# Performance work log

Measured on AMD Instinct MI355X. Metric: run time of the kernel, lower is better.

## Reference

```python
import jax, jax.numpy as jnp
import numpy as np

DIM = 512
SEQ_LEN = 1279
IMG = 32
K = 7
DIL = 1
H = 8
DH = 64
INNER = H * DH


def _unfold(x, k, pad, dil, pad_value=0.0):
    # x: [B, C, Hh, Ww] -> [B, Hh*Ww, k*k, C]  (torch F.unfold channel order: c outer, kernel inner)
    B, C, Hh, Ww = x.shape
    xp = jnp.pad(x, ((0, 0), (0, 0), (pad, pad), (pad, pad)), constant_values=pad_value)
    cols = [xp[:, :, i * dil:i * dil + Hh, j * dil:j * dil + Ww]
            for i in range(k) for j in range(k)]
    p = jnp.stack(cols, axis=2)  # [B, C, k*k, Hh, Ww]
    return p.reshape(B, C, k * k, Hh * Ww).transpose(0, 3, 2, 1)


def setup_inputs() -> dict:
    key = jax.random.key(0)
    ks = jax.random.split(key, 3)
    b = 4
    x = jax.random.normal(ks[0], (b, SEQ_LEN, DIM), jnp.float32)
    mask = jnp.ones((b, 256), dtype=bool)
    W_qkv = jax.random.normal(ks[1], (DIM, INNER * 3), jnp.float32) * 0.02
    W_out = jax.random.normal(ks[2], (INNER, DIM), jnp.float32) * 0.02
    b_out = jnp.zeros((DIM,), jnp.float32)
    return {"x": x, "mask": mask, "W_qkv": W_qkv, "W_out": W_out, "b_out": b_out}


def reference(x, mask, W_qkv, W_out, b_out):
    b, n, _ = x.shape
    img_seq_len = IMG * IMG                      # 1024
    text_len = SEQ_LEN + 1 - img_seq_len         # 256
    pad_n = SEQ_LEN - n + 1                      # pad to seq_len + 1
    scale = DH ** -0.5

    xp = jnp.pad(x, ((0, 0), (0, pad_n), (0, 0)))
    mask = mask[:, :text_len]

    qkv = xp @ W_qkv
    q, k, v = jnp.split(qkv, 3, axis=-1)

    def split_heads(t):
        B, N, _ = t.shape
        return t.reshape(B, N, H, DH).transpose(0, 2, 1, 3).reshape(B * H, N, DH)

    q, k, v = map(split_heads, (q, k, v))
    q = q * scale

    q_text, q_img = q[:, :-img_seq_len], q[:, -img_seq_len:]
    k_text, k_img = k[:, :-img_seq_len], k[:, -img_seq_len:]
    v_text, v_img = v[:, :-img_seq_len], v[:, -img_seq_len:]

    # --- text-to-text causal attention ---
    dots_text = jnp.einsum('bid,bjd->bij', q_text, k_text)
    mask_value = -jnp.finfo(dots_text.dtype).max
    i, j = dots_text.shape[-2:]
    causal_text = jnp.triu(jnp.ones((i, j), dtype=bool), j - i + 1)
    dots_text = jnp.where(causal_text, mask_value, dots_text)
    attn_text = jax.nn.softmax(dots_text, axis=-1)
    out_text = jnp.einsum('bij,bjd->bid', attn_text, v_text)

    # --- image local windowed attention (unfold) + image-to-text ---
    eff = (K - 1) * DIL + 1
    pad = eff // 2

    def to_img(t):
        B = t.shape[0]
        return t.transpose(0, 2, 1).reshape(B, DH, IMG, IMG)

    k_imgu = _unfold(to_img(k_img), K, pad, DIL)  # [BH, HW, KK, DH]
    v_imgu = _unfold(to_img(v_img), K, pad, DIL)

    dots_image = jnp.einsum('bid,bijd->bij', q_img, k_imgu)
    dots_i2t = jnp.einsum('bid,bjd->bij', q_img, k_text)

    img_seq = jnp.arange(img_seq_len, dtype=jnp.float32).reshape(1, 1, IMG, IMG)
    k_idx = _unfold(img_seq, K, pad, DIL, pad_value=float(img_seq_len))[..., 0]  # [1, HW, KK]
    q_idx = jnp.arange(img_seq_len)[None, :, None]
    causal_img = q_idx < k_idx  # [1, HW, KK]

    bh = q.shape[0]
    causal_img = jnp.broadcast_to(causal_img, (bh, img_seq_len, K * K))
    tmask = jnp.broadcast_to(mask[:, None, None, :], (b, H, img_seq_len, text_len)).reshape(bh, img_seq_len, text_len)
    full_mask = jnp.concatenate((~tmask, causal_img), axis=-1)

    dots = jnp.concatenate((dots_i2t, dots_image), axis=-1)
    dots = jnp.where(full_mask, mask_value, dots)
    attn = jax.nn.softmax(dots, axis=-1)
    attn_i2t, attn_img = attn[..., :text_len], attn[..., text_len:]

    out_img = (jnp.einsum('bij,bijd->bid', attn_img, v_imgu)
               + jnp.einsum('bij,bjd->bid', attn_i2t, v_text))

    out = jnp.concatenate((out_text, out_img), axis=1)  # [BH, N, DH]
    N = out.shape[1]
    out = out.reshape(b, H, N, DH).transpose(0, 2, 1, 3).reshape(b, N, INNER)
    out = out @ W_out + b_out
    return out[:, :n]
```

## Files before the change

kernel.cpp:

```cpp
#include <hip/hip_runtime.h>
#include <math.h>

#define DIMD 512
#define SEQ 1280
#define NREAL 1279
#define NTEXT 256
#define NIMG 1024
#define IMGW 32
#define NH 8
#define DH 64
#define BH 32
#define BATCH 4
#define VTW 1344
#define FLTMAX 3.402823466e38f

typedef __attribute__((ext_vector_type(8))) short short8;
typedef __attribute__((ext_vector_type(4))) float f32x4;
typedef __attribute__((ext_vector_type(4))) unsigned short ushort4v;
typedef __attribute__((ext_vector_type(8))) unsigned short ushort8v;

#define MFMA16(a, b, c) __builtin_amdgcn_mfma_f32_16x16x32_bf16((a), (b), (c), 0, 0, 0)

__device__ __forceinline__ unsigned short f2bf(float x) {
    unsigned int u = __builtin_bit_cast(unsigned int, x);
    u += 0x7fffu + ((u >> 16) & 1u);
    return (unsigned short)(u >> 16);
}

__device__ __forceinline__ void gload16(const unsigned short* g, unsigned short* l) {
    __builtin_amdgcn_global_load_lds(
        (const __attribute__((address_space(1))) unsigned int*)g,
        (__attribute__((address_space(3))) unsigned int*)l,
        16, 0, 0);
}

__global__ __launch_bounds__(256) void convert_fused(
    const float* __restrict__ x, const float* __restrict__ Wqkv,
    const float* __restrict__ Wout, unsigned short* __restrict__ xb,
    unsigned short* __restrict__ wqkvt, unsigned short* __restrict__ woutt)
{
    __shared__ unsigned short lds[64 * 65];
    const int blk = blockIdx.x;
    const int t = threadIdx.x;

    if (blk < 1280) {
        const size_t tt = (size_t)blk * 256 + t;
        const size_t e0 = tt * 8;
        const int row = (int)(e0 >> 9);
        const int d = (int)(e0 & 511);
        const int b = row / SEQ;
        const int ns = row - b * SEQ;
        ushort8v o;
        if (ns < NREAL) {
            const float4* p = reinterpret_cast<const float4*>(
                x + ((size_t)b * NREAL + ns) * DIMD + d);
            float4 v0 = p[0], v1 = p[1];
            o[0] = f2bf(v0.x); o[1] = f2bf(v0.y); o[2] = f2bf(v0.z); o[3] = f2bf(v0.w);
            o[4] = f2bf(v1.x); o[5] = f2bf(v1.y); o[6] = f2bf(v1.z); o[7] = f2bf(v1.w);
        } else {
            o = ushort8v{0, 0, 0, 0, 0, 0, 0, 0};
        }
        *reinterpret_cast<ushort8v*>(xb + e0) = o;
        return;
    }

    const bool isq = (blk < 1472);
    const int lb = blk - (isq ? 1280 : 1472);
    const float* W = isq ? Wqkv : Wout;
    unsigned short* Wt = isq ? wqkvt : woutt;
    const int N = isq ? 1536 : 512;
    const int k0 = (lb & 7) * 64, n0 = (lb >> 3) * 64;

    #pragma unroll
    for (int i = 0; i < 4; i++) {
        int idx = t + 256 * i;
        int r = idx >> 4, c4 = (idx & 15) * 4;
        float4 v = *reinterpret_cast<const float4*>(W + (size_t)(k0 + r) * N + n0 + c4);
        lds[(c4 + 0) * 65 + r] = f2bf(v.x);
        lds[(c4 + 1) * 65 + r] = f2bf(v.y);
        lds[(c4 + 2) * 65 + r] = f2bf(v.z);
        lds[(c4 + 3) * 65 + r] = f2bf(v.w);
    }
    __syncthreads();
    #pragma unroll
    for (int i = 0; i < 4; i++) {
        int idx = t + 256 * i;
        int n = idx >> 4, k4 = (idx & 15) * 4;
        ushort4v o;
        #pragma unroll
        for (int j = 0; j < 4; j++) o[j] = lds[n * 65 + k4 + j];
        *reinterpret_cast<ushort4v*>(Wt + (size_t)(n0 + n) * 512 + k0 + k4) = o;
    }
}

template<int TM, int TN, int EPI>
__global__ __launch_bounds__(256) void mfma_gemm(
    const unsigned short* __restrict__ A, const unsigned short* __restrict__ Bt,
    unsigned short* __restrict__ qb, unsigned short* __restrict__ kb,
    unsigned short* __restrict__ vt,
    const float* __restrict__ bias, float* __restrict__ out)
{
    constexpr int MI = TM / 32;
    constexpr int NI = TN / 32;
    __shared__ __align__(16) unsigned short As[TM * 64];
    __shared__ __align__(16) unsigned short Bs[TN * 64];
    const int tid = threadIdx.x;
    const int lane = tid & 63, w = tid >> 6;
    const int wm = w >> 1, wn = w & 1;
    const int g = lane >> 4, col = lane & 15;
    const int m0 = blockIdx.x * TM, n0 = blockIdx.y * TN;
    char* AsB = (char*)&As[0];
    char* BsB = (char*)&Bs[0];

    f32x4 acc[MI][NI] = {};

    for (int ks = 0; ks < 8; ks++) {
        const int k0 = ks * 64;
        #pragma unroll
        for (int j = 0; j < TM / 32; j++) {
            int rbase = w * (TM / 4) + j * 8;
            int r = rbase + (lane >> 3);
            int cs = (lane & 7) ^ (r & 7);
            gload16(A + (size_t)(m0 + r) * 512 + k0 + cs * 8,
                    (unsigned short*)(AsB + rbase * 128));
        }
        #pragma unroll
        for (int j = 0; j < TN / 32; j++) {
            int rbase = w * (TN / 4) + j * 8;
            int r = rbase + (lane >> 3);
            int cs = (lane & 7) ^ (r & 7);
            gload16(Bt + (size_t)(n0 + r) * 512 + k0 + cs * 8,
                    (unsigned short*)(BsB + rbase * 128));
        }
        __syncthreads();

        short8 af[MI][2], bfr[NI][2];
        #pragma unroll
        for (int mi = 0; mi < MI; mi++) {
            int rA = wm * (TM / 2) + mi * 16 + col;
            #pragma unroll
            for (int kk = 0; kk < 2; kk++) {
                int sl = (kk * 4 + g) ^ (rA & 7);
                af[mi][kk] = *reinterpret_cast<const short8*>(AsB + rA * 128 + sl * 16);
            }
        }
        #pragma unroll
        for (int ni = 0; ni < NI; ni++) {
            int rB = wn * (TN / 2) + ni * 16 + col;
            #pragma unroll
            for (int kk = 0; kk < 2; kk++) {
                int sl = (kk * 4 + g) ^ (rB & 7);
                bfr[ni][kk] = *reinterpret_cast<const short8*>(BsB + rB * 128 + sl * 16);
            }
        }
        #pragma unroll
        for (int kk = 0; kk < 2; kk++)
            #pragma unroll
            for (int mi = 0; mi < MI; mi++)
                #pragma unroll
                for (int ni = 0; ni < NI; ni++)
                    acc[mi][ni] = MFMA16(af[mi][kk], bfr[ni][kk], acc[mi][ni]);
        __syncthreads();
    }

    const int b = m0 / SEQ;
    const int nb = m0 - b * SEQ;

    if (EPI == 0) {
        #pragma unroll
        for (int ni = 0; ni < NI; ni++) {
            const int n = n0 + wn * (TN / 2) + ni * 16 + col;
            const int which = n >> 9;
            const int h = (n >> 6) & 7;
            const int dh = n & 63;
            const int bh = b * NH + h;
            #pragma unroll
            for (int mi = 0; mi < MI; mi++) {
                const int ns0 = nb + wm * (TM / 2) + mi * 16 + 4 * g;
                if (which == 2) {
                    ushort4v pk;
                    #pragma unroll
                    for (int rr = 0; rr < 4; rr++) pk[rr] = f2bf(acc[mi][ni][rr]);
                    *reinterpret_cast<ushort4v*>(
                        vt + ((size_t)bh * DH + dh) * VTW + ns0) = pk;
                } else {
                    unsigned short* dst = which ? kb : qb;
                    const float sc = which ? 1.f : 0.125f;
                    #pragma unroll
                    for (int rr = 0; rr < 4; rr++)
                        dst[((size_t)bh * SEQ + ns0 + rr) * DH + dh] =
                            f2bf(acc[mi][ni][rr] * sc);
                }
            }
        }
    } else {
        #pragma unroll
        for (int ni = 0; ni < NI; ni++) {
            const int n = n0 + wn * (TN / 2) + ni * 16 + col;
            const float bv = bias[n];
            #pragma unroll
            for (int mi = 0; mi < MI; mi++) {
                const int ns0 = nb + wm * (TM / 2) + mi * 16 + 4 * g;
                #pragma unroll
                for (int rr = 0; rr < 4; rr++) {
                    int ns = ns0 + rr;
                    if (ns < NREAL)
                        out[((size_t)b * NREAL + ns) * DIMD + n] = acc[mi][ni][rr] + bv;
                }
            }
        }
    }
}

__device__ __forceinline__ void attn_text_body(
    const unsigned short* __restrict__ qb, const unsigned short* __restrict__ kb,
    const unsigned short* __restrict__ vt, unsigned short* __restrict__ ao,
    unsigned short* P, int bh, int t, int lane)
{
    const int g = lane >> 4, col = lane & 15;
    const int b = bh >> 3, h = bh & 7;

    const size_t qrow = (size_t)bh * SEQ + t * 16 + col;
    const short8 qa0 = *reinterpret_cast<const short8*>(qb + qrow * DH + g * 8);
    const short8 qa1 = *reinterpret_cast<const short8*>(qb + qrow * DH + 32 + g * 8);

    f32x4 st[16];
    #pragma unroll
    for (int kt = 0; kt < 16; kt++) {
        if (kt <= t) {
            size_t krow = (size_t)bh * SEQ + kt * 16 + col;
            short8 kb0 = *reinterpret_cast<const short8*>(kb + krow * DH + g * 8);
            short8 kb1 = *reinterpret_cast<const short8*>(kb + krow * DH + 32 + g * 8);
            f32x4 s = {0.f, 0.f, 0.f, 0.f};
            s = MFMA16(qa0, kb0, s);
            s = MFMA16(qa1, kb1, s);
            if (kt == t) {
                #pragma unroll
                for (int rr = 0; rr < 4; rr++)
                    if (col > 4 * g + rr) s[rr] = -FLTMAX;
            }
            st[kt] = s;
        }
    }

    float m[4] = {-FLTMAX, -FLTMAX, -FLTMAX, -FLTMAX};
    #pragma unroll
    for (int kt = 0; kt < 16; kt++)
        if (kt <= t)
            #pragma unroll
            for (int rr = 0; rr < 4; rr++) m[rr] = fmaxf(m[rr], st[kt][rr]);
    #pragma unroll
    for (int rr = 0; rr < 4; rr++) {
        m[rr] = fmaxf(m[rr], __shfl_xor(m[rr], 1));
        m[rr] = fmaxf(m[rr], __shfl_xor(m[rr], 2));
        m[rr] = fmaxf(m[rr], __shfl_xor(m[rr], 4));
        m[rr] = fmaxf(m[rr], __shfl_xor(m[rr], 8));
    }
    float ssum[4] = {0.f, 0.f, 0.f, 0.f};
    #pragma unroll
    for (int kt = 0; kt < 16; kt++)
        if (kt <= t) {
            #pragma unroll
            for (int rr = 0; rr < 4; rr++) {
                float e = __expf(st[kt][rr] - m[rr]);
                st[kt][rr] = e;
                ssum[rr] += e;
            }
        }
    #pragma unroll
    for (int rr = 0; rr < 4; rr++) {
        ssum[rr] += __shfl_xor(ssum[rr], 1);
        ssum[rr] += __shfl_xor(ssum[rr], 2);
        ssum[rr] += __shfl_xor(ssum[rr], 4);
        ssum[rr] += __shfl_xor(ssum[rr], 8);
    }

    #pragma unroll
    for (int kt = 0; kt < 16; kt++)
        if (kt <= t) {
            #pragma unroll
            for (int rr = 0; rr < 4; rr++)
                P[(4 * g + rr) * 264 + kt * 16 + col] = f2bf(st[kt][rr]);
        }
    if ((t & 1) == 0) {
        ushort4v z = {0, 0, 0, 0};
        *reinterpret_cast<ushort4v*>(
            &P[(lane >> 2) * 264 + (t + 1) * 16 + (lane & 3) * 4]) = z;
    }
    __syncthreads();

    f32x4 acc[4] = {};
    #pragma unroll
    for (int kkb = 0; kkb < 8; kkb++) {
        if (kkb <= (t >> 1)) {
            short8 pa = *reinterpret_cast<const short8*>(&P[col * 264 + kkb * 32 + g * 8]);
            #pragma unroll
            for (int n0t = 0; n0t < 4; n0t++) {
                short8 vb = *reinterpret_cast<const short8*>(
                    vt + ((size_t)bh * DH + n0t * 16 + col) * VTW + kkb * 32 + g * 8);
                acc[n0t] = MFMA16(pa, vb, acc[n0t]);
            }
        }
    }

    #pragma unroll
    for (int rr = 0; rr < 4; rr++) {
        int qrow_o = t * 16 + 4 * g + rr;
        float inv = 1.f / ssum[rr];
        #pragma unroll
        for (int n0t = 0; n0t < 4; n0t++)
            ao[((size_t)b * SEQ + qrow_o) * DIMD + h * DH + n0t * 16 + col] =
                f2bf(acc[n0t][rr] * inv);
    }
}

__device__ __forceinline__ void attn_img_body(
    const unsigned short* __restrict__ qb, const unsigned short* __restrict__ kb,
    const unsigned short* __restrict__ vt, const int* __restrict__ mask,
    unsigned short* __restrict__ ao, unsigned short* P, int bh, int tile, int lane)
{
    const int r = tile >> 1, c0 = (tile & 1) << 4;
    const int g = lane >> 4, col = lane & 15;
    const int b = bh >> 3, h = bh & 7;

    const size_t qrow = (size_t)bh * SEQ + NTEXT + r * 32 + c0 + col;
    const short8 qa0 = *reinterpret_cast<const short8*>(qb + qrow * DH + g * 8);
    const short8 qa1 = *reinterpret_cast<const short8*>(qb + qrow * DH + 32 + g * 8);

    f32x4 st[16];
    #pragma unroll
    for (int kt = 0; kt < 16; kt++) {
        int j = kt * 16 + col;
        size_t krow = (size_t)bh * SEQ + j;
        short8 kb0 = *reinterpret_cast<const short8*>(kb + krow * DH + g * 8);
        short8 kb1 = *reinterpret_cast<const short8*>(kb + krow * DH + 32 + g * 8);
        f32x4 s = {0.f, 0.f, 0.f, 0.f};
        s = MFMA16(qa0, kb0, s);
        s = MFMA16(qa1, kb1, s);
        if (mask[b * 256 + j] == 0) {
            #pragma unroll
            for (int rr = 0; rr < 4; rr++) s[rr] = -FLTMAX;
        }
        st[kt] = s;
    }

    f32x4 sw[4][2];
    bool wvalid[4];
    #pragma unroll
    for (int w = 0; w < 4; w++) {
        int nr = r - 3 + w;
        wvalid[w] = (nr >= 0);
        if (nr >= 0) {
            #pragma unroll
            for (int ct = 0; ct < 2; ct++) {
                int nc = c0 - 8 + ct * 16 + col;
                int ncc = min(max(nc, 0), IMGW - 1);
                size_t krow = (size_t)bh * SEQ + NTEXT + nr * IMGW + ncc;
                short8 kb0 = *reinterpret_cast<const short8*>(kb + krow * DH + g * 8);
                short8 kb1 = *reinterpret_cast<const short8*>(kb + krow * DH + 32 + g * 8);
                f32x4 s = {0.f, 0.f, 0.f, 0.f};
                s = MFMA16(qa0, kb0, s);
                s = MFMA16(qa1, kb1, s);
                #pragma unroll
                for (int rr = 0; rr < 4; rr++) {
                    int q = 4 * g + rr;
                    int dnc = nc - (c0 + q);
                    bool ok = (nc >= 0) && (nc < IMGW) && (dnc >= -3) &&
                              (dnc <= ((w == 3) ? 0 : 3));
                    if (!ok) s[rr] = -FLTMAX;
                }
                sw[w][ct] = s;
            }
        }
    }

    float m[4] = {-FLTMAX, -FLTMAX, -FLTMAX, -FLTMAX};
    #pragma unroll
    for (int kt = 0; kt < 16; kt++)
        #pragma unroll
        for (int rr = 0; rr < 4; rr++) m[rr] = fmaxf(m[rr], st[kt][rr]);
    #pragma unroll
    for (int w = 0; w < 4; w++)
        if (wvalid[w])
            #pragma unroll
            for (int ct = 0; ct < 2; ct++)
                #pragma unroll
                for (int rr = 0; rr < 4; rr++) m[rr] = fmaxf(m[rr], sw[w][ct][rr]);
    #pragma unroll
    for (int rr = 0; rr < 4; rr++) {
        m[rr] = fmaxf(m[rr], __shfl_xor(m[rr], 1));
        m[rr] = fmaxf(m[rr], __shfl_xor(m[rr], 2));
        m[rr] = fmaxf(m[rr], __shfl_xor(m[rr], 4));
        m[rr] = fmaxf(m[rr], __shfl_xor(m[rr], 8));
    }
    float ssum[4] = {0.f, 0.f, 0.f, 0.f};
    #pragma unroll
    for (int kt = 0; kt < 16; kt++)
        #pragma unroll
        for (int rr = 0; rr < 4; rr++) {
            float e = __expf(st[kt][rr] - m[rr]);
            st[kt][rr] = e;
            ssum[rr] += e;
        }
    #pragma unroll
    for (int w = 0; w < 4; w++)
        if (wvalid[w])
            #pragma unroll
            for (int ct = 0; ct < 2; ct++)
                #pragma unroll
                for (int rr = 0; rr < 4; rr++) {
                    float e = __expf(sw[w][ct][rr] - m[rr]);
                    sw[w][ct][rr] = e;
                    ssum[rr] += e;
                }
    #pragma unroll
    for (int rr = 0; rr < 4; rr++) {
        ssum[rr] += __shfl_xor(ssum[rr], 1);
        ssum[rr] += __shfl_xor(ssum[rr], 2);
        ssum[rr] += __shfl_xor(ssum[rr], 4);
        ssum[rr] += __shfl_xor(ssum[rr], 8);
    }

    #pragma unroll
    for (int kt = 0; kt < 16; kt++)
        #pragma unroll
        for (int rr = 0; rr < 4; rr++)
            P[(4 * g + rr) * 392 + kt * 16 + col] = f2bf(st[kt][rr]);
    #pragma unroll
    for (int w = 0; w < 4; w++)
        if (wvalid[w])
            #pragma unroll
            for (int ct = 0; ct < 2; ct++)
                #pragma unroll
                for (int rr = 0; rr < 4; rr++)
                    P[(4 * g + rr) * 392 + 256 + w * 32 + ct * 16 + col] =
                        f2bf(sw[w][ct][rr]);
    __syncthreads();

    f32x4 acc[4] = {};
    #pragma unroll
    for (int kkb = 0; kkb < 8; kkb++) {
        short8 pa = *reinterpret_cast<const short8*>(&P[col * 392 + kkb * 32 + g * 8]);
        #pragma unroll
        for (int n0t = 0; n0t < 4; n0t++) {
            short8 vb = *reinterpret_cast<const short8*>(
                vt + ((size_t)bh * DH + n0t * 16 + col) * VTW + kkb * 32 + g * 8);
            acc[n0t] = MFMA16(pa, vb, acc[n0t]);
        }
    }
    #pragma unroll
    for (int w = 0; w < 4; w++) {
        if (wvalid[w]) {
            int nr = r - 3 + w;
            short8 pa = *reinterpret_cast<const short8*>(&P[col * 392 + 256 + w * 32 + g * 8]);
            size_t vkey = (size_t)(NTEXT + nr * IMGW + c0 - 8 + g * 8);
            #pragma unroll
            for (int n0t = 0; n0t < 4; n0t++) {
                short8 vb = *reinterpret_cast<const short8*>(
                    vt + ((size_t)bh * DH + n0t * 16 + col) * VTW + vkey);
                acc[n0t] = MFMA16(pa, vb, acc[n0t]);
            }
        }
    }

    #pragma unroll
    for (int rr = 0; rr < 4; rr++) {
        int qrow_o = NTEXT + r * IMGW + c0 + 4 * g + rr;
        float inv = 1.f / ssum[rr];
        #pragma unroll
        for (int n0t = 0; n0t < 4; n0t++)
            ao[((size_t)b * SEQ + qrow_o) * DIMD + h * DH + n0t * 16 + col] =
                f2bf(acc[n0t][rr] * inv);
    }
}

__global__ __launch_bounds__(64) void attn_fused(
    const unsigned short* __restrict__ qb, const unsigned short* __restrict__ kb,
    const unsigned short* __restrict__ vt, const int* __restrict__ mask,
    unsigned short* __restrict__ ao)
{
    __shared__ __align__(16) unsigned short P[16 * 392];
    const int blk = blockIdx.x;
    const int lane = threadIdx.x;
    if (blk < 512) {
        attn_text_body(qb, kb, vt, ao, P, blk >> 4, blk & 15, lane);
    } else {
        const int u = blk - 512;
        attn_img_body(qb, kb, vt, mask, ao, P, u >> 6, u & 63, lane);
    }
}

extern "C" void kernel_launch(void* const* d_in, const int* in_sizes, int n_in,
                              void* d_out, int out_size, void* d_ws, size_t ws_size,
                              hipStream_t stream) {
    const float* x    = (const float*)d_in[0];
    const int* mask   = (const int*)d_in[1];
    const float* Wqkv = (const float*)d_in[2];
    const float* Wout = (const float*)d_in[3];
    const float* bout = (const float*)d_in[4];
    float* out = (float*)d_out;

    unsigned short* ws = (unsigned short*)d_ws;
    const size_t XB  = (size_t)5120 * 512;
    const size_t WQT = (size_t)1536 * 512;
    const size_t WOT = (size_t)512 * 512;
    const size_t PER = (size_t)BH * SEQ * DH;
    const size_t VTE = (size_t)BH * DH * VTW;
    unsigned short* xb    = ws;
    unsigned short* wqkvt = xb + XB;
    unsigned short* woutt = wqkvt + WQT;
    unsigned short* qb    = woutt + WOT;
    unsigned short* kb    = qb + PER;
    unsigned short* vt    = kb + PER;
    unsigned short* ao    = vt + VTE;

    convert_fused<<<dim3(1536), dim3(256), 0, stream>>>(
        x, Wqkv, Wout, xb, wqkvt, woutt);
    mfma_gemm<64, 128, 0><<<dim3(80, 12), dim3(256), 0, stream>>>(
        xb, wqkvt, qb, kb, vt, nullptr, nullptr);
    attn_fused<<<dim3(2560), dim3(64), 0, stream>>>(qb, kb, vt, mask, ao);
    mfma_gemm<64, 64, 1><<<dim3(80, 8), dim3(256), 0, stream>>>(
        ao, woutt, nullptr, nullptr, nullptr, bout, out);
}
```

Before: 131.1 us.

## Split attention keys across two waves per block with flash-style merge

Each attention block now runs two wavefronts, each owning interleaved key tiles (even/odd 16-key tiles and half of the neighborhood window rows). Each wave computes its own partial softmax max, sum and PV accumulator, and the two are merged through shared memory with exp rescaling before a vectorized bf16 store. The aim is more parallelism and shorter per-wave serial chains in the attention kernel. The cost is extra LDS traffic, a block barrier and the rescale work.

Result: no change. 130.7 us (-0.3%).

```diff
diff --git a/kernel.cpp b/kernel.cpp
--- a/kernel.cpp
+++ b/kernel.cpp
@@ -12,6 +12,7 @@
 #define BH 32
 #define BATCH 4
 #define VTW 1344
+#define PSTR 200
 #define FLTMAX 3.402823466e38f
 
 typedef __attribute__((ext_vector_type(8))) short short8;
@@ -212,282 +213,280 @@
     }
 }
 
-__device__ __forceinline__ void attn_text_body(
-    const unsigned short* __restrict__ qb, const unsigned short* __restrict__ kb,
-    const unsigned short* __restrict__ vt, unsigned short* __restrict__ ao,
-    unsigned short* P, int bh, int t, int lane)
-{
-    const int g = lane >> 4, col = lane & 15;
-    const int b = bh >> 3, h = bh & 7;
-
-    const size_t qrow = (size_t)bh * SEQ + t * 16 + col;
-    const short8 qa0 = *reinterpret_cast<const short8*>(qb + qrow * DH + g * 8);
-    const short8 qa1 = *reinterpret_cast<const short8*>(qb + qrow * DH + 32 + g * 8);
-
-    f32x4 st[16];
-    #pragma unroll
-    for (int kt = 0; kt < 16; kt++) {
-        if (kt <= t) {
-            size_t krow = (size_t)bh * SEQ + kt * 16 + col;
-            short8 kb0 = *reinterpret_cast<const short8*>(kb + krow * DH + g * 8);
-            short8 kb1 = *reinterpret_cast<const short8*>(kb + krow * DH + 32 + g * 8);
-            f32x4 s = {0.f, 0.f, 0.f, 0.f};
-            s = MFMA16(qa0, kb0, s);
-            s = MFMA16(qa1, kb1, s);
-            if (kt == t) {
-                #pragma unroll
-                for (int rr = 0; rr < 4; rr++)
-                    if (col > 4 * g + rr) s[rr] = -FLTMAX;
-            }
-            st[kt] = s;
-        }
-    }
-
-    float m[4] = {-FLTMAX, -FLTMAX, -FLTMAX, -FLTMAX};
-    #pragma unroll
-    for (int kt = 0; kt < 16; kt++)
-        if (kt <= t)
-            #pragma unroll
-            for (int rr = 0; rr < 4; rr++) m[rr] = fmaxf(m[rr], st[kt][rr]);
-    #pragma unroll
-    for (int rr = 0; rr < 4; rr++) {
-        m[rr] = fmaxf(m[rr], __shfl_xor(m[rr], 1));
-        m[rr] = fmaxf(m[rr], __shfl_xor(m[rr], 2));
-        m[rr] = fmaxf(m[rr], __shfl_xor(m[rr], 4));
-        m[rr] = fmaxf(m[rr], __shfl_xor(m[rr], 8));
-    }
-    float ssum[4] = {0.f, 0.f, 0.f, 0.f};
-    #pragma unroll
-    for (int kt = 0; kt < 16; kt++)
-        if (kt <= t) {
-            #pragma unroll
-            for (int rr = 0; rr < 4; rr++) {
-                float e = __expf(st[kt][rr] - m[rr]);
-                st[kt][rr] = e;
-                ssum[rr] += e;
-            }
-        }
-    #pragma unroll
-    for (int rr = 0; rr < 4; rr++) {
-        ssum[rr] += __shfl_xor(ssum[rr], 1);
-        ssum[rr] += __shfl_xor(ssum[rr], 2);
-        ssum[rr] += __shfl_xor(ssum[rr], 4);
-        ssum[rr] += __shfl_xor(ssum[rr], 8);
-    }
-
-    #pragma unroll
-    for (int kt = 0; kt < 16; kt++)
-        if (kt <= t) {
-            #pragma unroll
-            for (int rr = 0; rr < 4; rr++)
-                P[(4 * g + rr) * 264 + kt * 16 + col] = f2bf(st[kt][rr]);
-        }
-    if ((t & 1) == 0) {
-        ushort4v z = {0, 0, 0, 0};
-        *reinterpret_cast<ushort4v*>(
-            &P[(lane >> 2) * 264 + (t + 1) * 16 + (lane & 3) * 4]) = z;
-    }
-    __syncthreads();
-
-    f32x4 acc[4] = {};
-    #pragma unroll
-    for (int kkb = 0; kkb < 8; kkb++) {
-        if (kkb <= (t >> 1)) {
-            short8 pa = *reinterpret_cast<const short8*>(&P[col * 264 + kkb * 32 + g * 8]);
-            #pragma unroll
-            for (int n0t = 0; n0t < 4; n0t++) {
-                short8 vb = *reinterpret_cast<const short8*>(
-                    vt + ((size_t)bh * DH + n0t * 16 + col) * VTW + kkb * 32 + g * 8);
-                acc[n0t] = MFMA16(pa, vb, acc[n0t]);
-            }
-        }
-    }
-
-    #pragma unroll
-    for (int rr = 0; rr < 4; rr++) {
-        int qrow_o = t * 16 + 4 * g + rr;
-        float inv = 1.f / ssum[rr];
-        #pragma unroll
-        for (int n0t = 0; n0t < 4; n0t++)
-            ao[((size_t)b * SEQ + qrow_o) * DIMD + h * DH + n0t * 16 + col] =
-                f2bf(acc[n0t][rr] * inv);
-    }
-}
-
-__device__ __forceinline__ void attn_img_body(
-    const unsigned short* __restrict__ qb, const unsigned short* __restrict__ kb,
-    const unsigned short* __restrict__ vt, const int* __restrict__ mask,
-    unsigned short* __restrict__ ao, unsigned short* P, int bh, int tile, int lane)
-{
-    const int r = tile >> 1, c0 = (tile & 1) << 4;
-    const int g = lane >> 4, col = lane & 15;
-    const int b = bh >> 3, h = bh & 7;
-
-    const size_t qrow = (size_t)bh * SEQ + NTEXT + r * 32 + c0 + col;
-    const short8 qa0 = *reinterpret_cast<const short8*>(qb + qrow * DH + g * 8);
-    const short8 qa1 = *reinterpret_cast<const short8*>(qb + qrow * DH + 32 + g * 8);
-
-    f32x4 st[16];
-    #pragma unroll
-    for (int kt = 0; kt < 16; kt++) {
-        int j = kt * 16 + col;
-        size_t krow = (size_t)bh * SEQ + j;
-        short8 kb0 = *reinterpret_cast<const short8*>(kb + krow * DH + g * 8);
-        short8 kb1 = *reinterpret_cast<const short8*>(kb + krow * DH + 32 + g * 8);
-        f32x4 s = {0.f, 0.f, 0.f, 0.f};
-        s = MFMA16(qa0, kb0, s);
-        s = MFMA16(qa1, kb1, s);
-        if (mask[b * 256 + j] == 0) {
-            #pragma unroll
-            for (int rr = 0; rr < 4; rr++) s[rr] = -FLTMAX;
-        }
-        st[kt] = s;
-    }
-
-    f32x4 sw[4][2];
-    bool wvalid[4];
-    #pragma unroll
-    for (int w = 0; w < 4; w++) {
-        int nr = r - 3 + w;
-        wvalid[w] = (nr >= 0);
-        if (nr >= 0) {
-            #pragma unroll
-            for (int ct = 0; ct < 2; ct++) {
-                int nc = c0 - 8 + ct * 16 + col;
-                int ncc = min(max(nc, 0), IMGW - 1);
-                size_t krow = (size_t)bh * SEQ + NTEXT + nr * IMGW + ncc;
-                short8 kb0 = *reinterpret_cast<const short8*>(kb + krow * DH + g * 8);
-                short8 kb1 = *reinterpret_cast<const short8*>(kb + krow * DH + 32 + g * 8);
-                f32x4 s = {0.f, 0.f, 0.f, 0.f};
-                s = MFMA16(qa0, kb0, s);
-                s = MFMA16(qa1, kb1, s);
-                #pragma unroll
-                for (int rr = 0; rr < 4; rr++) {
-                    int q = 4 * g + rr;
-                    int dnc = nc - (c0 + q);
-                    bool ok = (nc >= 0) && (nc < IMGW) && (dnc >= -3) &&
-                              (dnc <= ((w == 3) ? 0 : 3));
-                    if (!ok) s[rr] = -FLTMAX;
-                }
-                sw[w][ct] = s;
-            }
-        }
-    }
-
-    float m[4] = {-FLTMAX, -FLTMAX, -FLTMAX, -FLTMAX};
-    #pragma unroll
-    for (int kt = 0; kt < 16; kt++)
-        #pragma unroll
-        for (int rr = 0; rr < 4; rr++) m[rr] = fmaxf(m[rr], st[kt][rr]);
-    #pragma unroll
-    for (int w = 0; w < 4; w++)
-        if (wvalid[w])
-            #pragma unroll
-            for (int ct = 0; ct < 2; ct++)
-                #pragma unroll
-                for (int rr = 0; rr < 4; rr++) m[rr] = fmaxf(m[rr], sw[w][ct][rr]);
-    #pragma unroll
-    for (int rr = 0; rr < 4; rr++) {
-        m[rr] = fmaxf(m[rr], __shfl_xor(m[rr], 1));
-        m[rr] = fmaxf(m[rr], __shfl_xor(m[rr], 2));
-        m[rr] = fmaxf(m[rr], __shfl_xor(m[rr], 4));
-        m[rr] = fmaxf(m[rr], __shfl_xor(m[rr], 8));
-    }
-    float ssum[4] = {0.f, 0.f, 0.f, 0.f};
-    #pragma unroll
-    for (int kt = 0; kt < 16; kt++)
-        #pragma unroll
-        for (int rr = 0; rr < 4; rr++) {
-            float e = __expf(st[kt][rr] - m[rr]);
-            st[kt][rr] = e;
-            ssum[rr] += e;
-        }
-    #pragma unroll
-    for (int w = 0; w < 4; w++)
-        if (wvalid[w])
-            #pragma unroll
-            for (int ct = 0; ct < 2; ct++)
-                #pragma unroll
-                for (int rr = 0; rr < 4; rr++) {
-                    float e = __expf(sw[w][ct][rr] - m[rr]);
-                    sw[w][ct][rr] = e;
-                    ssum[rr] += e;
-                }
-    #pragma unroll
-    for (int rr = 0; rr < 4; rr++) {
-        ssum[rr] += __shfl_xor(ssum[rr], 1);
-        ssum[rr] += __shfl_xor(ssum[rr], 2);
-        ssum[rr] += __shfl_xor(ssum[rr], 4);
-        ssum[rr] += __shfl_xor(ssum[rr], 8);
-    }
-
-    #pragma unroll
-    for (int kt = 0; kt < 16; kt++)
-        #pragma unroll
-        for (int rr = 0; rr < 4; rr++)
-            P[(4 * g + rr) * 392 + kt * 16 + col] = f2bf(st[kt][rr]);
-    #pragma unroll
-    for (int w = 0; w < 4; w++)
-        if (wvalid[w])
-            #pragma unroll
-            for (int ct = 0; ct < 2; ct++)
-                #pragma unroll
-                for (int rr = 0; rr < 4; rr++)
-                    P[(4 * g + rr) * 392 + 256 + w * 32 + ct * 16 + col] =
-                        f2bf(sw[w][ct][rr]);
-    __syncthreads();
-
-    f32x4 acc[4] = {};
-    #pragma unroll
-    for (int kkb = 0; kkb < 8; kkb++) {
-        short8 pa = *reinterpret_cast<const short8*>(&P[col * 392 + kkb * 32 + g * 8]);
-        #pragma unroll
-        for (int n0t = 0; n0t < 4; n0t++) {
-            short8 vb = *reinterpret_cast<const short8*>(
-                vt + ((size_t)bh * DH + n0t * 16 + col) * VTW + kkb * 32 + g * 8);
-            acc[n0t] = MFMA16(pa, vb, acc[n0t]);
-        }
-    }
-    #pragma unroll
-    for (int w = 0; w < 4; w++) {
-        if (wvalid[w]) {
-            int nr = r - 3 + w;
-            short8 pa = *reinterpret_cast<const short8*>(&P[col * 392 + 256 + w * 32 + g * 8]);
-            size_t vkey = (size_t)(NTEXT + nr * IMGW + c0 - 8 + g * 8);
-            #pragma unroll
-            for (int n0t = 0; n0t < 4; n0t++) {
-                short8 vb = *reinterpret_cast<const short8*>(
-                    vt + ((size_t)bh * DH + n0t * 16 + col) * VTW + vkey);
-                acc[n0t] = MFMA16(pa, vb, acc[n0t]);
-            }
-        }
-    }
-
-    #pragma unroll
-    for (int rr = 0; rr < 4; rr++) {
-        int qrow_o = NTEXT + r * IMGW + c0 + 4 * g + rr;
-        float inv = 1.f / ssum[rr];
-        #pragma unroll
-        for (int n0t = 0; n0t < 4; n0t++)
-            ao[((size_t)b * SEQ + qrow_o) * DIMD + h * DH + n0t * 16 + col] =
-                f2bf(acc[n0t][rr] * inv);
-    }
-}
-
-__global__ __launch_bounds__(64) void attn_fused(
+__global__ __launch_bounds__(128) void attn_split(
     const unsigned short* __restrict__ qb, const unsigned short* __restrict__ kb,
     const unsigned short* __restrict__ vt, const int* __restrict__ mask,
     unsigned short* __restrict__ ao)
 {
-    __shared__ __align__(16) unsigned short P[16 * 392];
+    __shared__ __align__(16) unsigned short P[2][16 * PSTR];
+    __shared__ float OB[2][16][64];
+    __shared__ float OM[2][16];
+    __shared__ float OS[2][16];
+
     const int blk = blockIdx.x;
-    const int lane = threadIdx.x;
+    const int tid = threadIdx.x;
+    const int wid = tid >> 6, lane = tid & 63;
+    const int g = lane >> 4, col = lane & 15;
+    unsigned short* Pw = &P[wid][0];
+
+    int bh, qbase;
+    float m[4] = {-FLTMAX, -FLTMAX, -FLTMAX, -FLTMAX};
+    float s[4] = {0.f, 0.f, 0.f, 0.f};
+    f32x4 acc[4] = {};
+
     if (blk < 512) {
-        attn_text_body(qb, kb, vt, ao, P, blk >> 4, blk & 15, lane);
+        bh = blk >> 4;
+        const int t = blk & 15;
+        qbase = t * 16;
+        const size_t qrow = (size_t)bh * SEQ + qbase + col;
+        const short8 qa0 = *reinterpret_cast<const short8*>(qb + qrow * DH + g * 8);
+        const short8 qa1 = *reinterpret_cast<const short8*>(qb + qrow * DH + 32 + g * 8);
+
+        const int nkt = (t >= wid) ? ((t - wid) >> 1) + 1 : 0;
+        f32x4 st[8];
+        #pragma unroll
+        for (int i = 0; i < 8; i++) {
+            int kt = 2 * i + wid;
+            if (i < nkt) {
+                size_t krow = (size_t)bh * SEQ + kt * 16 + col;
+                short8 kb0 = *reinterpret_cast<const short8*>(kb + krow * DH + g * 8);
+                short8 kb1 = *reinterpret_cast<const short8*>(kb + krow * DH + 32 + g * 8);
+                f32x4 sv = {0.f, 0.f, 0.f, 0.f};
+                sv = MFMA16(qa0, kb0, sv);
+                sv = MFMA16(qa1, kb1, sv);
+                if (kt == t) {
+                    #pragma unroll
+                    for (int rr = 0; rr < 4; rr++)
+                        if (col > 4 * g + rr) sv[rr] = -FLTMAX;
+                }
+                st[i] = sv;
+            }
+        }
+        #pragma unroll
+        for (int i = 0; i < 8; i++)
+            if (i < nkt)
+                #pragma unroll
+                for (int rr = 0; rr < 4; rr++) m[rr] = fmaxf(m[rr], st[i][rr]);
+        #pragma unroll
+        for (int rr = 0; rr < 4; rr++) {
+            m[rr] = fmaxf(m[rr], __shfl_xor(m[rr], 1));
+            m[rr] = fmaxf(m[rr], __shfl_xor(m[rr], 2));
+            m[rr] = fmaxf(m[rr], __shfl_xor(m[rr], 4));
+            m[rr] = fmaxf(m[rr], __shfl_xor(m[rr], 8));
+        }
+        #pragma unroll
+        for (int i = 0; i < 8; i++)
+            if (i < nkt) {
+                #pragma unroll
+                for (int rr = 0; rr < 4; rr++) {
+                    float e = __expf(st[i][rr] - m[rr]);
+                    st[i][rr] = e;
+                    s[rr] += e;
+                }
+            }
+        #pragma unroll
+        for (int rr = 0; rr < 4; rr++) {
+            s[rr] += __shfl_xor(s[rr], 1);
+            s[rr] += __shfl_xor(s[rr], 2);
+            s[rr] += __shfl_xor(s[rr], 4);
+            s[rr] += __shfl_xor(s[rr], 8);
+        }
+        #pragma unroll
+        for (int i = 0; i < 8; i++)
+            if (i < nkt)
+                #pragma unroll
+                for (int rr = 0; rr < 4; rr++)
+                    Pw[(4 * g + rr) * PSTR + i * 16 + col] = f2bf(st[i][rr]);
+        if (nkt & 1) {
+            ushort4v z = {0, 0, 0, 0};
+            *reinterpret_cast<ushort4v*>(
+                &Pw[(lane >> 2) * PSTR + nkt * 16 + (lane & 3) * 4]) = z;
+        }
+        const int nck = (nkt + 1) >> 1;
+        #pragma unroll
+        for (int ck = 0; ck < 4; ck++) {
+            if (ck < nck) {
+                short8 pa = *reinterpret_cast<const short8*>(
+                    Pw + col * PSTR + ck * 32 + g * 8);
+                const int key_base = ck * 64 + (g >> 1) * 32 + wid * 16 + (g & 1) * 8;
+                #pragma unroll
+                for (int n0t = 0; n0t < 4; n0t++) {
+                    short8 vb = *reinterpret_cast<const short8*>(
+                        vt + ((size_t)bh * DH + n0t * 16 + col) * VTW + key_base);
+                    acc[n0t] = MFMA16(pa, vb, acc[n0t]);
+                }
+            }
+        }
     } else {
         const int u = blk - 512;
-        attn_img_body(qb, kb, vt, mask, ao, P, u >> 6, u & 63, lane);
-    }
+        bh = u >> 6;
+        const int tile = u & 63;
+        const int r = tile >> 1, c0 = (tile & 1) << 4;
+        qbase = NTEXT + r * IMGW + c0;
+        const int b0 = bh >> 3;
+        const size_t qrow = (size_t)bh * SEQ + qbase + col;
+        const short8 qa0 = *reinterpret_cast<const short8*>(qb + qrow * DH + g * 8);
+        const short8 qa1 = *reinterpret_cast<const short8*>(qb + qrow * DH + 32 + g * 8);
+
+        f32x4 st[8];
+        #pragma unroll
+        for (int i = 0; i < 8; i++) {
+            int j = (2 * i + wid) * 16 + col;
+            size_t krow = (size_t)bh * SEQ + j;
+            short8 kb0 = *reinterpret_cast<const short8*>(kb + krow * DH + g * 8);
+            short8 kb1 = *reinterpret_cast<const short8*>(kb + krow * DH + 32 + g * 8);
+            f32x4 sv = {0.f, 0.f, 0.f, 0.f};
+            sv = MFMA16(qa0, kb0, sv);
+            sv = MFMA16(qa1, kb1, sv);
+            if (mask[b0 * 256 + j] == 0) {
+                #pragma unroll
+                for (int rr = 0; rr < 4; rr++) sv[rr] = -FLTMAX;
+            }
+            st[i] = sv;
+        }
+        f32x4 sw[2][2];
+        bool wv[2];
+        #pragma unroll
+        for (int wi = 0; wi < 2; wi++) {
+            const int wg = 2 * wid + wi;
+            const int nr = r - 3 + wg;
+            wv[wi] = (nr >= 0);
+            if (wv[wi]) {
+                #pragma unroll
+                for (int ct = 0; ct < 2; ct++) {
+                    int nc = c0 - 8 + ct * 16 + col;
+                    int ncc = min(max(nc, 0), IMGW - 1);
+                    size_t krow = (size_t)bh * SEQ + NTEXT + nr * IMGW + ncc;
+                    short8 kb0 = *reinterpret_cast<const short8*>(kb + krow * DH + g * 8);
+                    short8 kb1 = *reinterpret_cast<const short8*>(kb + krow * DH + 32 + g * 8);
+                    f32x4 sv = {0.f, 0.f, 0.f, 0.f};
+                    sv = MFMA16(qa0, kb0, sv);
+                    sv = MFMA16(qa1, kb1, sv);
+                    #pragma unroll
+                    for (int rr = 0; rr < 4; rr++) {
+                        int q = 4 * g + rr;
+                        int dnc = nc - (c0 + q);
+                        bool ok = (nc >= 0) && (nc < IMGW) && (dnc >= -3) &&
+                                  (dnc <= ((wg == 3) ? 0 : 3));
+                        if (!ok) sv[rr] = -FLTMAX;
+                    }
+                    sw[wi][ct] = sv;
+                }
+            }
+        }
+        #pragma unroll
+        for (int i = 0; i < 8; i++)
+            #pragma unroll
+            for (int rr = 0; rr < 4; rr++) m[rr] = fmaxf(m[rr], st[i][rr]);
+        #pragma unroll
+        for (int wi = 0; wi < 2; wi++)
+            if (wv[wi])
+                #pragma unroll
+                for (int ct = 0; ct < 2; ct++)
+                    #pragma unroll
+                    for (int rr = 0; rr < 4; rr++) m[rr] = fmaxf(m[rr], sw[wi][ct][rr]);
+        #pragma unroll
+        for (int rr = 0; rr < 4; rr++) {
+            m[rr] = fmaxf(m[rr], __shfl_xor(m[rr], 1));
+            m[rr] = fmaxf(m[rr], __shfl_xor(m[rr], 2));
+            m[rr] = fmaxf(m[rr], __shfl_xor(m[rr], 4));
+            m[rr] = fmaxf(m[rr], __shfl_xor(m[rr], 8));
+        }
+        #pragma unroll
+        for (int i = 0; i < 8; i++)
+            #pragma unroll
+            for (int rr = 0; rr < 4; rr++) {
+                float e = __expf(st[i][rr] - m[rr]);
+                st[i][rr] = e;
+                s[rr] += e;
+            }
+        #pragma unroll
+        for (int wi = 0; wi < 2; wi++)
+            if (wv[wi])
+                #pragma unroll
+                for (int ct = 0; ct < 2; ct++)
+                    #pragma unroll
+                    for (int rr = 0; rr < 4; rr++) {
+                        float e = __expf(sw[wi][ct][rr] - m[rr]);
+                        sw[wi][ct][rr] = e;
+                        s[rr] += e;
+                    }
+        #pragma unroll
+        for (int rr = 0; rr < 4; rr++) {
+            s[rr] += __shfl_xor(s[rr], 1);
+            s[rr] += __shfl_xor(s[rr], 2);
+            s[rr] += __shfl_xor(s[rr], 4);
+            s[rr] += __shfl_xor(s[rr], 8);
+        }
+        #pragma unroll
+        for (int i = 0; i < 8; i++)
+            #pragma unroll
+            for (int rr = 0; rr < 4; rr++)
+                Pw[(4 * g + rr) * PSTR + i * 16 + col] = f2bf(st[i][rr]);
+        #pragma unroll
+        for (int wi = 0; wi < 2; wi++)
+            if (wv[wi])
+                #pragma unroll
+                for (int ct = 0; ct < 2; ct++)
+                    #pragma unroll
+                    for (int rr = 0; rr < 4; rr++)
+                        Pw[(4 * g + rr) * PSTR + 128 + wi * 32 + ct * 16 + col] =
+                            f2bf(sw[wi][ct][rr]);
+        #pragma unroll
+        for (int ck = 0; ck < 4; ck++) {
+            short8 pa = *reinterpret_cast<const short8*>(
+                Pw + col * PSTR + ck * 32 + g * 8);
+            const int key_base = ck * 64 + (g >> 1) * 32 + wid * 16 + (g & 1) * 8;
+            #pragma unroll
+            for (int n0t = 0; n0t < 4; n0t++) {
+                short8 vb = *reinterpret_cast<const short8*>(
+                    vt + ((size_t)bh * DH + n0t * 16 + col) * VTW + key_base);
+                acc[n0t] = MFMA16(pa, vb, acc[n0t]);
+            }
+        }
+        #pragma unroll
+        for (int wi = 0; wi < 2; wi++) {
+            if (wv[wi]) {
+                const int nr = r - 3 + 2 * wid + wi;
+                short8 pa = *reinterpret_cast<const short8*>(
+                    Pw + col * PSTR + 128 + wi * 32 + g * 8);
+                const size_t vkey = (size_t)(NTEXT + nr * IMGW + c0 - 8 + g * 8);
+                #pragma unroll
+                for (int n0t = 0; n0t < 4; n0t++) {
+                    short8 vb = *reinterpret_cast<const short8*>(
+                        vt + ((size_t)bh * DH + n0t * 16 + col) * VTW + vkey);
+                    acc[n0t] = MFMA16(pa, vb, acc[n0t]);
+                }
+            }
+        }
+    }
+
+    #pragma unroll
+    for (int rr = 0; rr < 4; rr++) {
+        #pragma unroll
+        for (int n0t = 0; n0t < 4; n0t++)
+            OB[wid][4 * g + rr][n0t * 16 + col] = acc[n0t][rr];
+        if (col == 0) {
+            OM[wid][4 * g + rr] = m[rr];
+            OS[wid][4 * g + rr] = s[rr];
+        }
+    }
+    __syncthreads();
+
+    const int q = tid >> 3, d0 = (tid & 7) * 8;
+    const float m0 = OM[0][q], m1 = OM[1][q];
+    const float M = fmaxf(m0, m1);
+    const float f0 = __expf(m0 - M), f1 = __expf(m1 - M);
+    const float inv = 1.f / (OS[0][q] * f0 + OS[1][q] * f1);
+    ushort8v o;
+    #pragma unroll
+    for (int e = 0; e < 8; e++) {
+        float v = (OB[0][q][d0 + e] * f0 + OB[1][q][d0 + e] * f1) * inv;
+        o[e] = f2bf(v);
+    }
+    const int b = bh >> 3, h = bh & 7;
+    *reinterpret_cast<ushort8v*>(
+        ao + ((size_t)b * SEQ + qbase + q) * DIMD + h * DH + d0) = o;
 }
 
 extern "C" void kernel_launch(void* const* d_in, const int* in_sizes, int n_in,
@@ -518,7 +517,7 @@
         x, Wqkv, Wout, xb, wqkvt, woutt);
     mfma_gemm<64, 128, 0><<<dim3(80, 12), dim3(256), 0, stream>>>(
         xb, wqkvt, qb, kb, vt, nullptr, nullptr);
-    attn_fused<<<dim3(2560), dim3(64), 0, stream>>>(qb, kb, vt, mask, ao);
+    attn_split<<<dim3(2560), dim3(128), 0, stream>>>(qb, kb, vt, mask, ao);
     mfma_gemm<64, 64, 1><<<dim3(80, 8), dim3(256), 0, stream>>>(
         ao, woutt, nullptr, nullptr, nullptr, bout, out);
 }
```
